# Kernel tuning notes

Measured on AMD Instinct MI355X. Metric: run time of the kernel, lower is better.

Reference implementation:

```python
import jax, jax.numpy as jnp
import numpy as np

T, H, E, I, IS = 1024, 2048, 64, 512, 1024
TOP_K = 8
CAP = 256


def setup_inputs() -> dict:
    key = jax.random.key(0)
    ks = jax.random.split(key, 9)
    s = 0.02
    return {
        "hidden_states": jax.random.normal(ks[0], (T, H), jnp.float32),
        "gate_w": jax.random.normal(ks[1], (E, H), jnp.float32) * s,
        "w1": jax.random.normal(ks[2], (E, H, I), jnp.float32) * s,
        "w3": jax.random.normal(ks[3], (E, H, I), jnp.float32) * s,
        "w2": jax.random.normal(ks[4], (E, I, H), jnp.float32) * s,
        "ws1": jax.random.normal(ks[5], (H, IS), jnp.float32) * s,
        "ws3": jax.random.normal(ks[6], (H, IS), jnp.float32) * s,
        "ws2": jax.random.normal(ks[7], (IS, H), jnp.float32) * s,
        "wsg": jax.random.normal(ks[8], (H, 1), jnp.float32) * s,
    }


def reference(hidden_states, gate_w, w1, w3, w2, ws1, ws3, ws2, wsg):
    x = hidden_states  # [T, H]
    n_tok = x.shape[0]

    # ---- router (Renormalize: top-k over logits, softmax over selected) ----
    logits = x @ gate_w.T                                  # [T, E]
    top_vals, top_idx = jax.lax.top_k(logits, TOP_K)       # [T, k]
    route_w = jax.nn.softmax(top_vals, axis=-1)            # renormalized weights

    # ---- dispatch: flatten (token, slot) assignments, rank within expert ----
    e = top_idx.reshape(-1)                                # [T*k] expert ids
    t = jnp.repeat(jnp.arange(n_tok), TOP_K)               # [T*k] token ids
    w_flat = route_w.reshape(-1)
    order = jnp.argsort(e, stable=True)
    counts = jax.ops.segment_sum(jnp.ones_like(e), e, num_segments=E)
    starts = jnp.cumsum(counts) - counts                   # exclusive cumsum
    pos_sorted = jnp.arange(e.shape[0]) - starts[e[order]]
    pos = jnp.zeros_like(e).at[order].set(pos_sorted)      # rank within expert
    valid = pos < CAP
    slot = jnp.where(valid, e * CAP + pos, E * CAP)        # overflow -> dump slot

    buf = jnp.zeros((E * CAP + 1, x.shape[1]), x.dtype).at[slot].set(x[t])
    xb = buf[:-1].reshape(E, CAP, x.shape[1])              # [E, C, H]

    # ---- grouped SwiGLU experts ----
    g = jax.nn.silu(jnp.einsum('ech,ehi->eci', xb, w1))
    u = jnp.einsum('ech,ehi->eci', xb, w3)
    yb = jnp.einsum('eci,eih->ech', g * u, w2).reshape(E * CAP, -1)

    # ---- combine ----
    contrib = yb[jnp.minimum(slot, E * CAP - 1)] * (w_flat * valid)[:, None]
    routed = jnp.zeros_like(x).at[t].add(contrib)

    # ---- shared expert with sigmoid gate ----
    shared = (jax.nn.silu(x @ ws1) * (x @ ws3)) @ ws2
    shared = jax.nn.sigmoid(x @ wsg) * shared

    return routed + shared
```

## Files before the change

### kernel.cpp

```cpp
#include <hip/hip_runtime.h>
#include <hip/hip_bf16.h>

#define NT    1024
#define HDIM  2048
#define NEXP  64
#define IDIM  512
#define ISDIM 1024
#define KTOP  8
#define ECAP  256

typedef float  f32x4 __attribute__((ext_vector_type(4)));
typedef __bf16 bf16x8 __attribute__((ext_vector_type(8)));
typedef unsigned short u16x8 __attribute__((ext_vector_type(8)));

#define SWZ(r, q) ((((q) ^ ((r) & 3) ^ (((r) >> 2) & 3)) & 3) << 3)

static __device__ __forceinline__ unsigned short f2b(float f) {
  __hip_bfloat16 h = __float2bfloat16(f);
  return __builtin_bit_cast(unsigned short, h);
}
static __device__ __forceinline__ float b2f(unsigned short u) {
  return __bfloat162float(__builtin_bit_cast(__hip_bfloat16, u));
}
static __device__ __forceinline__ void sync_lds() {
  __builtin_amdgcn_s_waitcnt(0xc07f);
  __builtin_amdgcn_s_barrier();
}

__global__ __launch_bounds__(256) void k_router(
    const float* __restrict__ x, const float* __restrict__ gw,
    const float* __restrict__ wsg,
    int* __restrict__ counts, int* __restrict__ tok_list,
    int* __restrict__ slot_map, float* __restrict__ wgt_map,
    float* __restrict__ gate_sig)
{
  __shared__ float xs[HDIM];
  __shared__ float lg[NEXP];
  __shared__ float selv[KTOP];
  __shared__ int   sele[KTOP];
  const int t = blockIdx.x, tid = threadIdx.x;
  const float* xr = x + (size_t)t * HDIM;
  for (int i = tid; i < HDIM / 4; i += 256)
    ((f32x4*)xs)[i] = ((const f32x4*)xr)[i];
  __syncthreads();
  const int wave = tid >> 6, lane = tid & 63;
  for (int ei = 0; ei < 16; ++ei) {
    const int e = wave * 16 + ei;
    const float* g = gw + (size_t)e * HDIM;
    float s = 0.f;
    for (int j = lane; j < HDIM; j += 64) s += xs[j] * g[j];
    for (int off = 32; off; off >>= 1) s += __shfl_xor(s, off, 64);
    if (lane == 0) lg[e] = s;
  }
  if (wave == 1) {
    float s = 0.f;
    for (int j = lane; j < HDIM; j += 64) s += xs[j] * wsg[j];
    for (int off = 32; off; off >>= 1) s += __shfl_xor(s, off, 64);
    if (lane == 0) gate_sig[t] = 1.f / (1.f + __expf(-s));
  }
  __syncthreads();
  if (wave == 0) {
    float v = lg[lane];
    for (int k = 0; k < KTOP; ++k) {
      float m = v;
      for (int off = 32; off; off >>= 1) m = fmaxf(m, __shfl_xor(m, off, 64));
      unsigned long long msk = __ballot(v == m);
      int src = __ffsll(msk) - 1;
      if (lane == src) v = -3.4e38f;
      if (lane == 0) { selv[k] = m; sele[k] = src; }
    }
  }
  __syncthreads();
  if (tid < KTOP) {
    const int k = tid;
    const float mx = selv[0];
    float sum = 0.f;
    for (int i = 0; i < KTOP; ++i) sum += __expf(selv[i] - mx);
    const float w = __expf(selv[k] - mx) / sum;
    const int e = sele[k];
    const int pos = atomicAdd(&counts[e], 1);
    int slot = -1;
    if (pos < ECAP) { slot = e * ECAP + pos; tok_list[slot] = t; }
    slot_map[t * KTOP + k] = slot;
    wgt_map[t * KTOP + k] = w;
  }
}

__global__ __launch_bounds__(512, 2) void k_gemm1(
    const float* __restrict__ x,
    const float* __restrict__ w1, const float* __restrict__ w3,
    const float* __restrict__ ws1, const float* __restrict__ ws3,
    const int* __restrict__ counts, const int* __restrict__ tok_list,
    unsigned short* __restrict__ hbuf, unsigned short* __restrict__ hsbuf)
{
  __shared__ unsigned short lds[32768];
  const int cpx = gridDim.x >> 3;
  const int b0 = blockIdx.x;
  const int bid = (b0 & 7) * cpx + (b0 >> 3);
  const int tid = threadIdx.x;
  bool is_exp;
  int g, ntile, me, ldb, m0s = 0;
  const float *b1p, *b3p;
  if (bid < NEXP * 4) {
    is_exp = true; g = bid >> 2; ntile = bid & 3;
    me = counts[g]; me = me < ECAP ? me : ECAP;
    if (me == 0) return;
    ldb = IDIM;
  } else {
    is_exp = false;
    const int s = bid - NEXP * 4;
    g = s >> 3; ntile = s & 7;
    me = 256; ldb = ISDIM; m0s = g * 256;
  }
  const int n0 = ntile * 128;
  if (is_exp) {
    b1p = w1 + (size_t)g * HDIM * IDIM + n0;
    b3p = w3 + (size_t)g * HDIM * IDIM + n0;
  } else {
    b1p = ws1 + n0;
    b3p = ws3 + n0;
  }
  const int ar = tid & 255, sel = tid >> 8, kh = sel * 16;
  bool avalid;
  const float* arow;
  if (is_exp) {
    avalid = (ar < me);
    const int tok = avalid ? tok_list[g * ECAP + ar] : 0;
    arow = x + (size_t)tok * HDIM + kh;
  } else {
    avalid = true;
    arow = x + (size_t)(m0s + ar) * HDIM + kh;
  }
  const int aoff0 = ar * 32 + SWZ(ar, sel * 2);
  const int aoff1 = ar * 32 + SWZ(ar, sel * 2 + 1);
  const int bn = tid & 127, bg = tid >> 7;
  const float* b1c = b1p + (size_t)(bg * 8) * ldb + bn;
  const float* b3c = b3p + (size_t)(bg * 8) * ldb + bn;
  const int boffB = bn * 32 + SWZ(bn, bg);
  const int lane = tid & 63, quad = lane >> 4, l15 = lane & 15;
  const int wv = tid >> 6, wm = wv >> 1, wn = wv & 1;
  const bool wactive = (wm * 64 < me);
  int aro[4], bo[4];
#pragma unroll
  for (int i = 0; i < 4; ++i) {
    const int rr = wm * 64 + i * 16 + l15;
    aro[i] = rr * 32 + SWZ(rr, quad);
    const int nn = wn * 64 + i * 16 + l15;
    bo[i] = nn * 32 + SWZ(nn, quad);
  }
  f32x4 acc1[4][4], acc3[4][4];
#pragma unroll
  for (int i = 0; i < 4; ++i)
#pragma unroll
    for (int j = 0; j < 4; ++j) {
      acc1[i][j] = f32x4{0.f, 0.f, 0.f, 0.f};
      acc3[i][j] = f32x4{0.f, 0.f, 0.f, 0.f};
    }
  f32x4 arg[4];
  float b1v[8], b3v[8];
  const int KT = HDIM / 32;
  if (avalid) {
    arg[0] = ((const f32x4*)arow)[0]; arg[1] = ((const f32x4*)arow)[1];
    arg[2] = ((const f32x4*)arow)[2]; arg[3] = ((const f32x4*)arow)[3];
  }
#pragma unroll
  for (int j = 0; j < 8; ++j) {
    b1v[j] = b1c[(size_t)j * ldb];
    b3v[j] = b3c[(size_t)j * ldb];
  }

  for (int kt = 0; kt < KT; ++kt) {
    unsigned short* L = lds + (kt & 1) * 16384;
    if (avalid) {
      u16x8 p0, p1;
#pragma unroll
      for (int i = 0; i < 4; ++i) {
        p0[i] = f2b(arg[0][i]); p0[4 + i] = f2b(arg[1][i]);
        p1[i] = f2b(arg[2][i]); p1[4 + i] = f2b(arg[3][i]);
      }
      *(u16x8*)&L[aoff0] = p0;
      *(u16x8*)&L[aoff1] = p1;
    }
    {
      u16x8 pb1, pb3;
#pragma unroll
      for (int j = 0; j < 8; ++j) { pb1[j] = f2b(b1v[j]); pb3[j] = f2b(b3v[j]); }
      *(u16x8*)&L[8192 + boffB] = pb1;
      *(u16x8*)&L[12288 + boffB] = pb3;
    }
    if (kt + 1 < KT) {
      const float* ap = arow + (kt + 1) * 32;
      if (avalid) {
        arg[0] = ((const f32x4*)ap)[0]; arg[1] = ((const f32x4*)ap)[1];
        arg[2] = ((const f32x4*)ap)[2]; arg[3] = ((const f32x4*)ap)[3];
      }
      const float* p1 = b1c + (size_t)(kt + 1) * 32 * ldb;
      const float* p3 = b3c + (size_t)(kt + 1) * 32 * ldb;
#pragma unroll
      for (int j = 0; j < 8; ++j) {
        b1v[j] = p1[(size_t)j * ldb];
        b3v[j] = p3[(size_t)j * ldb];
      }
    }
    sync_lds();
    if (wactive) {
      bf16x8 af[4], bf1[4], bf3[4];
#pragma unroll
      for (int i = 0; i < 4; ++i)
        af[i] = __builtin_bit_cast(bf16x8, *(const u16x8*)&L[aro[i]]);
#pragma unroll
      for (int j = 0; j < 4; ++j) {
        bf1[j] = __builtin_bit_cast(bf16x8, *(const u16x8*)&L[8192 + bo[j]]);
        bf3[j] = __builtin_bit_cast(bf16x8, *(const u16x8*)&L[12288 + bo[j]]);
      }
#pragma unroll
      for (int i = 0; i < 4; ++i)
#pragma unroll
        for (int j = 0; j < 4; ++j) {
          acc1[i][j] = __builtin_amdgcn_mfma_f32_16x16x32_bf16(af[i], bf1[j], acc1[i][j], 0, 0, 0);
          acc3[i][j] = __builtin_amdgcn_mfma_f32_16x16x32_bf16(af[i], bf3[j], acc3[i][j], 0, 0, 0);
        }
    }
  }
  if (wactive) {
#pragma unroll
    for (int i = 0; i < 4; ++i) {
#pragma unroll
      for (int q = 0; q < 4; ++q) {
        const int rr = wm * 64 + i * 16 + quad * 4 + q;
        if (is_exp && rr >= me) continue;
        unsigned short* orow = is_exp
            ? hbuf + ((size_t)g * ECAP + rr) * IDIM
            : hsbuf + (size_t)(m0s + rr) * ISDIM;
#pragma unroll
        for (int j = 0; j < 4; ++j) {
          const int col = n0 + wn * 64 + j * 16 + l15;
          const float gg = acc1[i][j][q];
          const float uu = acc3[i][j][q];
          const float sv = (gg / (1.f + __expf(-gg))) * uu;
          orow[col] = f2b(sv);
        }
      }
    }
  }
}

__global__ __launch_bounds__(512, 2) void k_gemm2(
    const unsigned short* __restrict__ hbuf, const unsigned short* __restrict__ hsbuf,
    const float* __restrict__ w2, const float* __restrict__ ws2,
    const int* __restrict__ counts, const float* __restrict__ gate_sig,
    unsigned short* __restrict__ yb, float* __restrict__ out)
{
  __shared__ unsigned short lds[24576];
  const int cpx = gridDim.x >> 3;
  const int b0 = blockIdx.x;
  const int bid = (b0 & 7) * cpx + (b0 >> 3);
  const int tid = threadIdx.x;
  bool is_exp;
  int g, ntile, me, K, m0s = 0;
  const unsigned short* abase;
  const float* bbase;
  if (bid < NEXP * 16) {
    is_exp = true; g = bid >> 4; ntile = bid & 15;
    me = counts[g]; me = me < ECAP ? me : ECAP;
    if (me == 0) return;
    K = IDIM;
    abase = hbuf + (size_t)g * ECAP * IDIM;
  } else {
    is_exp = false;
    const int s = bid - NEXP * 16;
    g = s >> 4; ntile = s & 15;
    me = 256; K = ISDIM; m0s = g * 256;
    abase = hsbuf + (size_t)m0s * ISDIM;
  }
  const int n0 = ntile * 128;
  bbase = is_exp ? (w2 + (size_t)g * IDIM * HDIM + n0) : (ws2 + n0);
  const int ar = tid & 255, sel = tid >> 8, kh = sel * 16;
  const bool avalid = (ar < me);
  const unsigned short* arow = abase + (size_t)ar * K + kh;
  const int aoff0 = ar * 32 + SWZ(ar, sel * 2);
  const int aoff1 = ar * 32 + SWZ(ar, sel * 2 + 1);
  const int bn = tid & 127, bg = tid >> 7;
  const float* bc = bbase + (size_t)(bg * 8) * HDIM + bn;
  const int boffB = bn * 32 + SWZ(bn, bg);
  const int lane = tid & 63, quad = lane >> 4, l15 = lane & 15;
  const int wv = tid >> 6, wm = wv >> 1, wn = wv & 1;
  const bool wactive = (wm * 64 < me);
  int aro[4], bo[4];
#pragma unroll
  for (int i = 0; i < 4; ++i) {
    const int rr = wm * 64 + i * 16 + l15;
    aro[i] = rr * 32 + SWZ(rr, quad);
    const int nn = wn * 64 + i * 16 + l15;
    bo[i] = nn * 32 + SWZ(nn, quad);
  }
  f32x4 acc[4][4];
#pragma unroll
  for (int i = 0; i < 4; ++i)
#pragma unroll
    for (int j = 0; j < 4; ++j) acc[i][j] = f32x4{0.f, 0.f, 0.f, 0.f};
  u16x8 a0r, a1r;
  float bv[8];
  const int KT = K / 32;
  if (avalid) { a0r = ((const u16x8*)arow)[0]; a1r = ((const u16x8*)arow)[1]; }
#pragma unroll
  for (int j = 0; j < 8; ++j) bv[j] = bc[(size_t)j * HDIM];

  for (int kt = 0; kt < KT; ++kt) {
    unsigned short* L = lds + (kt & 1) * 12288;
    if (avalid) { *(u16x8*)&L[aoff0] = a0r; *(u16x8*)&L[aoff1] = a1r; }
    {
      u16x8 pb;
#pragma unroll
      for (int j = 0; j < 8; ++j) pb[j] = f2b(bv[j]);
      *(u16x8*)&L[8192 + boffB] = pb;
    }
    if (kt + 1 < KT) {
      const unsigned short* ap = arow + (kt + 1) * 32;
      if (avalid) { a0r = ((const u16x8*)ap)[0]; a1r = ((const u16x8*)ap)[1]; }
      const float* p = bc + (size_t)(kt + 1) * 32 * HDIM;
#pragma unroll
      for (int j = 0; j < 8; ++j) bv[j] = p[(size_t)j * HDIM];
    }
    sync_lds();
    if (wactive) {
      bf16x8 af[4], bfr[4];
#pragma unroll
      for (int i = 0; i < 4; ++i)
        af[i] = __builtin_bit_cast(bf16x8, *(const u16x8*)&L[aro[i]]);
#pragma unroll
      for (int j = 0; j < 4; ++j)
        bfr[j] = __builtin_bit_cast(bf16x8, *(const u16x8*)&L[8192 + bo[j]]);
#pragma unroll
      for (int i = 0; i < 4; ++i)
#pragma unroll
        for (int j = 0; j < 4; ++j)
          acc[i][j] = __builtin_amdgcn_mfma_f32_16x16x32_bf16(af[i], bfr[j], acc[i][j], 0, 0, 0);
    }
  }
  if (wactive) {
#pragma unroll
    for (int i = 0; i < 4; ++i) {
#pragma unroll
      for (int q = 0; q < 4; ++q) {
        const int rr = wm * 64 + i * 16 + quad * 4 + q;
        if (is_exp) {
          if (rr >= me) continue;
          unsigned short* orow = yb + ((size_t)g * ECAP + rr) * HDIM;
#pragma unroll
          for (int j = 0; j < 4; ++j) {
            const int col = n0 + wn * 64 + j * 16 + l15;
            orow[col] = f2b(acc[i][j][q]);
          }
        } else {
          const float gt = gate_sig[m0s + rr];
          float* orow = out + (size_t)(m0s + rr) * HDIM;
#pragma unroll
          for (int j = 0; j < 4; ++j) {
            const int col = n0 + wn * 64 + j * 16 + l15;
            orow[col] = gt * acc[i][j][q];
          }
        }
      }
    }
  }
}

__global__ __launch_bounds__(256) void k_combine(
    const unsigned short* __restrict__ yb,
    const int* __restrict__ slot_map, const float* __restrict__ wgt_map,
    float* __restrict__ out)
{
  __shared__ int ss[KTOP];
  __shared__ float ww[KTOP];
  const int t = blockIdx.x, tid = threadIdx.x;
  if (tid < KTOP) { ss[tid] = slot_map[t * KTOP + tid]; ww[tid] = wgt_map[t * KTOP + tid]; }
  __syncthreads();
  const int c = tid * 8;
  float* op = out + (size_t)t * HDIM + c;
  f32x4 o0 = ((const f32x4*)op)[0];
  f32x4 o1 = ((const f32x4*)op)[1];
  for (int k = 0; k < KTOP; ++k) {
    const int s = ss[k];
    if (s < 0) continue;
    const float w = ww[k];
    const u16x8 y = *(const u16x8*)(yb + (size_t)s * HDIM + c);
#pragma unroll
    for (int i = 0; i < 4; ++i) {
      o0[i] += w * b2f(y[i]);
      o1[i] += w * b2f(y[4 + i]);
    }
  }
  ((f32x4*)op)[0] = o0;
  ((f32x4*)op)[1] = o1;
}

extern "C" void kernel_launch(void* const* d_in, const int* in_sizes, int n_in,
                              void* d_out, int out_size, void* d_ws, size_t ws_size,
                              hipStream_t stream) {
  (void)in_sizes; (void)n_in; (void)out_size; (void)ws_size;
  const float* x   = (const float*)d_in[0];
  const float* gw  = (const float*)d_in[1];
  const float* w1  = (const float*)d_in[2];
  const float* w3  = (const float*)d_in[3];
  const float* w2  = (const float*)d_in[4];
  const float* ws1 = (const float*)d_in[5];
  const float* ws3 = (const float*)d_in[6];
  const float* ws2 = (const float*)d_in[7];
  const float* wsg = (const float*)d_in[8];
  float* out = (float*)d_out;
  char* ws = (char*)d_ws;
  int*   counts   = (int*)ws;
  int*   tok_list = (int*)(ws + 256);
  int*   slot_map = (int*)(ws + 256 + (64 << 10));
  float* wgt_map  = (float*)(ws + 256 + (96 << 10));
  float* gate_sig = (float*)(ws + 256 + (128 << 10));
  unsigned short* hbuf  = (unsigned short*)(ws + (1 << 20));
  unsigned short* hsbuf = (unsigned short*)(ws + (17 << 20));
  unsigned short* yb    = (unsigned short*)(ws + (19 << 20));

  hipMemsetAsync(counts, 0, 256, stream);
  k_router<<<dim3(NT), dim3(256), 0, stream>>>(x, gw, wsg, counts, tok_list,
                                               slot_map, wgt_map, gate_sig);
  k_gemm1<<<dim3(NEXP * 4 + 32), dim3(512), 0, stream>>>(x, w1, w3, ws1, ws3,
                                                         counts, tok_list, hbuf, hsbuf);
  k_gemm2<<<dim3(NEXP * 16 + 64), dim3(512), 0, stream>>>(hbuf, hsbuf, w2, ws2,
                                                          counts, gate_sig, yb, out);
  k_combine<<<dim3(NT), dim3(256), 0, stream>>>(yb, slot_map, wgt_map, out);
}
```

Before: 1.099 ms.

## Shrink GEMM tiles to 128x128 and split experts across M tiles

Both grouped GEMM kernels move from 256-row M tiles to 128-row tiles. Experts are split into two M tiles, and tiles that are entirely empty exit early. Warps are rearranged 2x4 and LDS use is halved, and launch bounds now target 4 blocks per CU for higher occupancy and more blocks. The cost is that each weight tile is streamed twice per expert (once per M tile) when the expert has more than 128 tokens, and per-MFMA register reuse is lower.

```diff
diff --git a/kernel.cpp b/kernel.cpp
--- a/kernel.cpp
+++ b/kernel.cpp
@@ -86,170 +86,12 @@
   }
 }
 
-__global__ __launch_bounds__(512, 2) void k_gemm1(
+__global__ __launch_bounds__(512, 4) void k_gemm1(
     const float* __restrict__ x,
     const float* __restrict__ w1, const float* __restrict__ w3,
     const float* __restrict__ ws1, const float* __restrict__ ws3,
     const int* __restrict__ counts, const int* __restrict__ tok_list,
     unsigned short* __restrict__ hbuf, unsigned short* __restrict__ hsbuf)
-{
-  __shared__ unsigned short lds[32768];
-  const int cpx = gridDim.x >> 3;
-  const int b0 = blockIdx.x;
-  const int bid = (b0 & 7) * cpx + (b0 >> 3);
-  const int tid = threadIdx.x;
-  bool is_exp;
-  int g, ntile, me, ldb, m0s = 0;
-  const float *b1p, *b3p;
-  if (bid < NEXP * 4) {
-    is_exp = true; g = bid >> 2; ntile = bid & 3;
-    me = counts[g]; me = me < ECAP ? me : ECAP;
-    if (me == 0) return;
-    ldb = IDIM;
-  } else {
-    is_exp = false;
-    const int s = bid - NEXP * 4;
-    g = s >> 3; ntile = s & 7;
-    me = 256; ldb = ISDIM; m0s = g * 256;
-  }
-  const int n0 = ntile * 128;
-  if (is_exp) {
-    b1p = w1 + (size_t)g * HDIM * IDIM + n0;
-    b3p = w3 + (size_t)g * HDIM * IDIM + n0;
-  } else {
-    b1p = ws1 + n0;
-    b3p = ws3 + n0;
-  }
-  const int ar = tid & 255, sel = tid >> 8, kh = sel * 16;
-  bool avalid;
-  const float* arow;
-  if (is_exp) {
-    avalid = (ar < me);
-    const int tok = avalid ? tok_list[g * ECAP + ar] : 0;
-    arow = x + (size_t)tok * HDIM + kh;
-  } else {
-    avalid = true;
-    arow = x + (size_t)(m0s + ar) * HDIM + kh;
-  }
-  const int aoff0 = ar * 32 + SWZ(ar, sel * 2);
-  const int aoff1 = ar * 32 + SWZ(ar, sel * 2 + 1);
-  const int bn = tid & 127, bg = tid >> 7;
-  const float* b1c = b1p + (size_t)(bg * 8) * ldb + bn;
-  const float* b3c = b3p + (size_t)(bg * 8) * ldb + bn;
-  const int boffB = bn * 32 + SWZ(bn, bg);
-  const int lane = tid & 63, quad = lane >> 4, l15 = lane & 15;
-  const int wv = tid >> 6, wm = wv >> 1, wn = wv & 1;
-  const bool wactive = (wm * 64 < me);
-  int aro[4], bo[4];
-#pragma unroll
-  for (int i = 0; i < 4; ++i) {
-    const int rr = wm * 64 + i * 16 + l15;
-    aro[i] = rr * 32 + SWZ(rr, quad);
-    const int nn = wn * 64 + i * 16 + l15;
-    bo[i] = nn * 32 + SWZ(nn, quad);
-  }
-  f32x4 acc1[4][4], acc3[4][4];
-#pragma unroll
-  for (int i = 0; i < 4; ++i)
-#pragma unroll
-    for (int j = 0; j < 4; ++j) {
-      acc1[i][j] = f32x4{0.f, 0.f, 0.f, 0.f};
-      acc3[i][j] = f32x4{0.f, 0.f, 0.f, 0.f};
-    }
-  f32x4 arg[4];
-  float b1v[8], b3v[8];
-  const int KT = HDIM / 32;
-  if (avalid) {
-    arg[0] = ((const f32x4*)arow)[0]; arg[1] = ((const f32x4*)arow)[1];
-    arg[2] = ((const f32x4*)arow)[2]; arg[3] = ((const f32x4*)arow)[3];
-  }
-#pragma unroll
-  for (int j = 0; j < 8; ++j) {
-    b1v[j] = b1c[(size_t)j * ldb];
-    b3v[j] = b3c[(size_t)j * ldb];
-  }
-
-  for (int kt = 0; kt < KT; ++kt) {
-    unsigned short* L = lds + (kt & 1) * 16384;
-    if (avalid) {
-      u16x8 p0, p1;
-#pragma unroll
-      for (int i = 0; i < 4; ++i) {
-        p0[i] = f2b(arg[0][i]); p0[4 + i] = f2b(arg[1][i]);
-        p1[i] = f2b(arg[2][i]); p1[4 + i] = f2b(arg[3][i]);
-      }
-      *(u16x8*)&L[aoff0] = p0;
-      *(u16x8*)&L[aoff1] = p1;
-    }
-    {
-      u16x8 pb1, pb3;
-#pragma unroll
-      for (int j = 0; j < 8; ++j) { pb1[j] = f2b(b1v[j]); pb3[j] = f2b(b3v[j]); }
-      *(u16x8*)&L[8192 + boffB] = pb1;
-      *(u16x8*)&L[12288 + boffB] = pb3;
-    }
-    if (kt + 1 < KT) {
-      const float* ap = arow + (kt + 1) * 32;
-      if (avalid) {
-        arg[0] = ((const f32x4*)ap)[0]; arg[1] = ((const f32x4*)ap)[1];
-        arg[2] = ((const f32x4*)ap)[2]; arg[3] = ((const f32x4*)ap)[3];
-      }
-      const float* p1 = b1c + (size_t)(kt + 1) * 32 * ldb;
-      const float* p3 = b3c + (size_t)(kt + 1) * 32 * ldb;
-#pragma unroll
-      for (int j = 0; j < 8; ++j) {
-        b1v[j] = p1[(size_t)j * ldb];
-        b3v[j] = p3[(size_t)j * ldb];
-      }
-    }
-    sync_lds();
-    if (wactive) {
-      bf16x8 af[4], bf1[4], bf3[4];
-#pragma unroll
-      for (int i = 0; i < 4; ++i)
-        af[i] = __builtin_bit_cast(bf16x8, *(const u16x8*)&L[aro[i]]);
-#pragma unroll
-      for (int j = 0; j < 4; ++j) {
-        bf1[j] = __builtin_bit_cast(bf16x8, *(const u16x8*)&L[8192 + bo[j]]);
-        bf3[j] = __builtin_bit_cast(bf16x8, *(const u16x8*)&L[12288 + bo[j]]);
-      }
-#pragma unroll
-      for (int i = 0; i < 4; ++i)
-#pragma unroll
-        for (int j = 0; j < 4; ++j) {
-          acc1[i][j] = __builtin_amdgcn_mfma_f32_16x16x32_bf16(af[i], bf1[j], acc1[i][j], 0, 0, 0);
-          acc3[i][j] = __builtin_amdgcn_mfma_f32_16x16x32_bf16(af[i], bf3[j], acc3[i][j], 0, 0, 0);
-        }
-    }
-  }
-  if (wactive) {
-#pragma unroll
-    for (int i = 0; i < 4; ++i) {
-#pragma unroll
-      for (int q = 0; q < 4; ++q) {
-        const int rr = wm * 64 + i * 16 + quad * 4 + q;
-        if (is_exp && rr >= me) continue;
-        unsigned short* orow = is_exp
-            ? hbuf + ((size_t)g * ECAP + rr) * IDIM
-            : hsbuf + (size_t)(m0s + rr) * ISDIM;
-#pragma unroll
-        for (int j = 0; j < 4; ++j) {
-          const int col = n0 + wn * 64 + j * 16 + l15;
-          const float gg = acc1[i][j][q];
-          const float uu = acc3[i][j][q];
-          const float sv = (gg / (1.f + __expf(-gg))) * uu;
-          orow[col] = f2b(sv);
-        }
-      }
-    }
-  }
-}
-
-__global__ __launch_bounds__(512, 2) void k_gemm2(
-    const unsigned short* __restrict__ hbuf, const unsigned short* __restrict__ hsbuf,
-    const float* __restrict__ w2, const float* __restrict__ ws2,
-    const int* __restrict__ counts, const float* __restrict__ gate_sig,
-    unsigned short* __restrict__ yb, float* __restrict__ out)
 {
   __shared__ unsigned short lds[24576];
   const int cpx = gridDim.x >> 3;
@@ -257,85 +99,234 @@
   const int bid = (b0 & 7) * cpx + (b0 >> 3);
   const int tid = threadIdx.x;
   bool is_exp;
-  int g, ntile, me, K, m0s = 0;
+  int g = 0, ntile, mtile, me, ldb, m0;
+  const float *b1p, *b3p;
+  if (bid < NEXP * 8) {
+    is_exp = true;
+    g = bid >> 3; ntile = (bid >> 1) & 3; mtile = bid & 1;
+    me = counts[g]; me = me < ECAP ? me : ECAP;
+    m0 = mtile * 128;
+    if (m0 >= me) return;
+    ldb = IDIM;
+    b1p = w1 + (size_t)g * HDIM * IDIM + ntile * 128;
+    b3p = w3 + (size_t)g * HDIM * IDIM + ntile * 128;
+  } else {
+    is_exp = false;
+    const int s = bid - NEXP * 8;
+    ntile = s >> 3; mtile = s & 7;
+    me = NT; m0 = mtile * 128; ldb = ISDIM;
+    b1p = ws1 + ntile * 128;
+    b3p = ws3 + ntile * 128;
+  }
+  const int n0 = ntile * 128;
+  const int ar = tid & 127, sel = tid >> 7;
+  const bool avalid = (m0 + ar) < me;
+  const float* arow;
+  if (is_exp) {
+    const int tok = avalid ? tok_list[g * ECAP + m0 + ar] : 0;
+    arow = x + (size_t)tok * HDIM + sel * 8;
+  } else {
+    arow = x + (size_t)(m0 + ar) * HDIM + sel * 8;
+  }
+  const int aoff = ar * 32 + SWZ(ar, sel);
+  const int bn = tid & 127, bg = tid >> 7;
+  const float* b1c = b1p + (size_t)(bg * 8) * ldb + bn;
+  const float* b3c = b3p + (size_t)(bg * 8) * ldb + bn;
+  const int boffB = bn * 32 + SWZ(bn, bg);
+  const int lane = tid & 63, quad = lane >> 4, l15 = lane & 15;
+  const int wv = tid >> 6, wm = wv >> 2, wn = wv & 3;
+  const bool wactive = (m0 + wm * 64) < me;
+  int aro[4], bo[2];
+#pragma unroll
+  for (int i = 0; i < 4; ++i) {
+    const int rr = wm * 64 + i * 16 + l15;
+    aro[i] = rr * 32 + SWZ(rr, quad);
+  }
+#pragma unroll
+  for (int j = 0; j < 2; ++j) {
+    const int nn = wn * 32 + j * 16 + l15;
+    bo[j] = nn * 32 + SWZ(nn, quad);
+  }
+  f32x4 acc1[4][2], acc3[4][2];
+#pragma unroll
+  for (int i = 0; i < 4; ++i)
+#pragma unroll
+    for (int j = 0; j < 2; ++j) {
+      acc1[i][j] = f32x4{0.f, 0.f, 0.f, 0.f};
+      acc3[i][j] = f32x4{0.f, 0.f, 0.f, 0.f};
+    }
+  f32x4 a0, a1;
+  float b1v[8], b3v[8];
+  const int KT = HDIM / 32;
+  if (avalid) { a0 = ((const f32x4*)arow)[0]; a1 = ((const f32x4*)arow)[1]; }
+#pragma unroll
+  for (int j = 0; j < 8; ++j) {
+    b1v[j] = b1c[(size_t)j * ldb];
+    b3v[j] = b3c[(size_t)j * ldb];
+  }
+
+  for (int kt = 0; kt < KT; ++kt) {
+    unsigned short* L = lds + (kt & 1) * 12288;
+    if (avalid) {
+      u16x8 p;
+#pragma unroll
+      for (int i = 0; i < 4; ++i) { p[i] = f2b(a0[i]); p[4 + i] = f2b(a1[i]); }
+      *(u16x8*)&L[aoff] = p;
+    }
+    {
+      u16x8 pb1, pb3;
+#pragma unroll
+      for (int j = 0; j < 8; ++j) { pb1[j] = f2b(b1v[j]); pb3[j] = f2b(b3v[j]); }
+      *(u16x8*)&L[4096 + boffB] = pb1;
+      *(u16x8*)&L[8192 + boffB] = pb3;
+    }
+    if (kt + 1 < KT) {
+      const float* ap = arow + (kt + 1) * 32;
+      if (avalid) { a0 = ((const f32x4*)ap)[0]; a1 = ((const f32x4*)ap)[1]; }
+      const float* p1 = b1c + (size_t)(kt + 1) * 32 * ldb;
+      const float* p3 = b3c + (size_t)(kt + 1) * 32 * ldb;
+#pragma unroll
+      for (int j = 0; j < 8; ++j) {
+        b1v[j] = p1[(size_t)j * ldb];
+        b3v[j] = p3[(size_t)j * ldb];
+      }
+    }
+    sync_lds();
+    if (wactive) {
+      bf16x8 bf1[2], bf3[2];
+#pragma unroll
+      for (int j = 0; j < 2; ++j) {
+        bf1[j] = __builtin_bit_cast(bf16x8, *(const u16x8*)&L[4096 + bo[j]]);
+        bf3[j] = __builtin_bit_cast(bf16x8, *(const u16x8*)&L[8192 + bo[j]]);
+      }
+#pragma unroll
+      for (int i = 0; i < 4; ++i) {
+        const bf16x8 af = __builtin_bit_cast(bf16x8, *(const u16x8*)&L[aro[i]]);
+#pragma unroll
+        for (int j = 0; j < 2; ++j) {
+          acc1[i][j] = __builtin_amdgcn_mfma_f32_16x16x32_bf16(af, bf1[j], acc1[i][j], 0, 0, 0);
+          acc3[i][j] = __builtin_amdgcn_mfma_f32_16x16x32_bf16(af, bf3[j], acc3[i][j], 0, 0, 0);
+        }
+      }
+    }
+  }
+  if (wactive) {
+#pragma unroll
+    for (int i = 0; i < 4; ++i) {
+#pragma unroll
+      for (int q = 0; q < 4; ++q) {
+        const int rr = m0 + wm * 64 + i * 16 + quad * 4 + q;
+        if (rr >= me) continue;
+        unsigned short* orow = is_exp
+            ? hbuf + ((size_t)g * ECAP + rr) * IDIM
+            : hsbuf + (size_t)rr * ISDIM;
+#pragma unroll
+        for (int j = 0; j < 2; ++j) {
+          const int col = n0 + wn * 32 + j * 16 + l15;
+          const float gg = acc1[i][j][q];
+          const float uu = acc3[i][j][q];
+          const float sv = (gg / (1.f + __expf(-gg))) * uu;
+          orow[col] = f2b(sv);
+        }
+      }
+    }
+  }
+}
+
+__global__ __launch_bounds__(512, 4) void k_gemm2(
+    const unsigned short* __restrict__ hbuf, const unsigned short* __restrict__ hsbuf,
+    const float* __restrict__ w2, const float* __restrict__ ws2,
+    const int* __restrict__ counts, const float* __restrict__ gate_sig,
+    unsigned short* __restrict__ yb, float* __restrict__ out)
+{
+  __shared__ unsigned short lds[16384];
+  const int cpx = gridDim.x >> 3;
+  const int b0 = blockIdx.x;
+  const int bid = (b0 & 7) * cpx + (b0 >> 3);
+  const int tid = threadIdx.x;
+  bool is_exp;
+  int g = 0, ntile, mtile, me, K, m0;
   const unsigned short* abase;
   const float* bbase;
-  if (bid < NEXP * 16) {
-    is_exp = true; g = bid >> 4; ntile = bid & 15;
+  if (bid < NEXP * 32) {
+    is_exp = true;
+    g = bid >> 5; ntile = (bid >> 1) & 15; mtile = bid & 1;
     me = counts[g]; me = me < ECAP ? me : ECAP;
-    if (me == 0) return;
+    m0 = mtile * 128;
+    if (m0 >= me) return;
     K = IDIM;
     abase = hbuf + (size_t)g * ECAP * IDIM;
+    bbase = w2 + (size_t)g * IDIM * HDIM + ntile * 128;
   } else {
     is_exp = false;
-    const int s = bid - NEXP * 16;
-    g = s >> 4; ntile = s & 15;
-    me = 256; K = ISDIM; m0s = g * 256;
-    abase = hsbuf + (size_t)m0s * ISDIM;
+    const int s = bid - NEXP * 32;
+    ntile = s >> 3; mtile = s & 7;
+    me = NT; m0 = mtile * 128; K = ISDIM;
+    abase = hsbuf;
+    bbase = ws2 + ntile * 128;
   }
   const int n0 = ntile * 128;
-  bbase = is_exp ? (w2 + (size_t)g * IDIM * HDIM + n0) : (ws2 + n0);
-  const int ar = tid & 255, sel = tid >> 8, kh = sel * 16;
-  const bool avalid = (ar < me);
-  const unsigned short* arow = abase + (size_t)ar * K + kh;
-  const int aoff0 = ar * 32 + SWZ(ar, sel * 2);
-  const int aoff1 = ar * 32 + SWZ(ar, sel * 2 + 1);
+  const int ar = tid & 127, sel = tid >> 7;
+  const bool avalid = (m0 + ar) < me;
+  const unsigned short* arow = abase + (size_t)(avalid ? (m0 + ar) : 0) * K + sel * 8;
+  const int aoff = ar * 32 + SWZ(ar, sel);
   const int bn = tid & 127, bg = tid >> 7;
   const float* bc = bbase + (size_t)(bg * 8) * HDIM + bn;
   const int boffB = bn * 32 + SWZ(bn, bg);
   const int lane = tid & 63, quad = lane >> 4, l15 = lane & 15;
-  const int wv = tid >> 6, wm = wv >> 1, wn = wv & 1;
-  const bool wactive = (wm * 64 < me);
-  int aro[4], bo[4];
+  const int wv = tid >> 6, wm = wv >> 2, wn = wv & 3;
+  const bool wactive = (m0 + wm * 64) < me;
+  int aro[4], bo[2];
 #pragma unroll
   for (int i = 0; i < 4; ++i) {
     const int rr = wm * 64 + i * 16 + l15;
     aro[i] = rr * 32 + SWZ(rr, quad);
-    const int nn = wn * 64 + i * 16 + l15;
-    bo[i] = nn * 32 + SWZ(nn, quad);
-  }
-  f32x4 acc[4][4];
+  }
+#pragma unroll
+  for (int j = 0; j < 2; ++j) {
+    const int nn = wn * 32 + j * 16 + l15;
+    bo[j] = nn * 32 + SWZ(nn, quad);
+  }
+  f32x4 acc[4][2];
 #pragma unroll
   for (int i = 0; i < 4; ++i)
 #pragma unroll
-    for (int j = 0; j < 4; ++j) acc[i][j] = f32x4{0.f, 0.f, 0.f, 0.f};
-  u16x8 a0r, a1r;
+    for (int j = 0; j < 2; ++j) acc[i][j] = f32x4{0.f, 0.f, 0.f, 0.f};
+  u16x8 a0r;
   float bv[8];
   const int KT = K / 32;
-  if (avalid) { a0r = ((const u16x8*)arow)[0]; a1r = ((const u16x8*)arow)[1]; }
+  if (avalid) a0r = *(const u16x8*)arow;
 #pragma unroll
   for (int j = 0; j < 8; ++j) bv[j] = bc[(size_t)j * HDIM];
 
   for (int kt = 0; kt < KT; ++kt) {
-    unsigned short* L = lds + (kt & 1) * 12288;
-    if (avalid) { *(u16x8*)&L[aoff0] = a0r; *(u16x8*)&L[aoff1] = a1r; }
+    unsigned short* L = lds + (kt & 1) * 8192;
+    if (avalid) *(u16x8*)&L[aoff] = a0r;
     {
       u16x8 pb;
 #pragma unroll
       for (int j = 0; j < 8; ++j) pb[j] = f2b(bv[j]);
-      *(u16x8*)&L[8192 + boffB] = pb;
+      *(u16x8*)&L[4096 + boffB] = pb;
     }
     if (kt + 1 < KT) {
-      const unsigned short* ap = arow + (kt + 1) * 32;
-      if (avalid) { a0r = ((const u16x8*)ap)[0]; a1r = ((const u16x8*)ap)[1]; }
+      if (avalid) a0r = *(const u16x8*)(arow + (kt + 1) * 32);
       const float* p = bc + (size_t)(kt + 1) * 32 * HDIM;
 #pragma unroll
       for (int j = 0; j < 8; ++j) bv[j] = p[(size_t)j * HDIM];
     }
     sync_lds();
     if (wactive) {
-      bf16x8 af[4], bfr[4];
-#pragma unroll
-      for (int i = 0; i < 4; ++i)
-        af[i] = __builtin_bit_cast(bf16x8, *(const u16x8*)&L[aro[i]]);
-#pragma unroll
-      for (int j = 0; j < 4; ++j)
-        bfr[j] = __builtin_bit_cast(bf16x8, *(const u16x8*)&L[8192 + bo[j]]);
-#pragma unroll
-      for (int i = 0; i < 4; ++i)
-#pragma unroll
-        for (int j = 0; j < 4; ++j)
-          acc[i][j] = __builtin_amdgcn_mfma_f32_16x16x32_bf16(af[i], bfr[j], acc[i][j], 0, 0, 0);
+      bf16x8 bfr[2];
+#pragma unroll
+      for (int j = 0; j < 2; ++j)
+        bfr[j] = __builtin_bit_cast(bf16x8, *(const u16x8*)&L[4096 + bo[j]]);
+#pragma unroll
+      for (int i = 0; i < 4; ++i) {
+        const bf16x8 af = __builtin_bit_cast(bf16x8, *(const u16x8*)&L[aro[i]]);
+#pragma unroll
+        for (int j = 0; j < 2; ++j)
+          acc[i][j] = __builtin_amdgcn_mfma_f32_16x16x32_bf16(af, bfr[j], acc[i][j], 0, 0, 0);
+      }
     }
   }
   if (wactive) {
@@ -343,21 +334,21 @@
     for (int i = 0; i < 4; ++i) {
 #pragma unroll
       for (int q = 0; q < 4; ++q) {
-        const int rr = wm * 64 + i * 16 + quad * 4 + q;
+        const int rr = m0 + wm * 64 + i * 16 + quad * 4 + q;
+        if (rr >= me) continue;
         if (is_exp) {
-          if (rr >= me) continue;
           unsigned short* orow = yb + ((size_t)g * ECAP + rr) * HDIM;
 #pragma unroll
-          for (int j = 0; j < 4; ++j) {
-            const int col = n0 + wn * 64 + j * 16 + l15;
+          for (int j = 0; j < 2; ++j) {
+            const int col = n0 + wn * 32 + j * 16 + l15;
             orow[col] = f2b(acc[i][j][q]);
           }
         } else {
-          const float gt = gate_sig[m0s + rr];
-          float* orow = out + (size_t)(m0s + rr) * HDIM;
-#pragma unroll
-          for (int j = 0; j < 4; ++j) {
-            const int col = n0 + wn * 64 + j * 16 + l15;
+          const float gt = gate_sig[rr];
+          float* orow = out + (size_t)rr * HDIM;
+#pragma unroll
+          for (int j = 0; j < 2; ++j) {
+            const int col = n0 + wn * 32 + j * 16 + l15;
             orow[col] = gt * acc[i][j][q];
           }
         }
@@ -422,9 +413,9 @@
   hipMemsetAsync(counts, 0, 256, stream);
   k_router<<<dim3(NT), dim3(256), 0, stream>>>(x, gw, wsg, counts, tok_list,
                                                slot_map, wgt_map, gate_sig);
-  k_gemm1<<<dim3(NEXP * 4 + 32), dim3(512), 0, stream>>>(x, w1, w3, ws1, ws3,
+  k_gemm1<<<dim3(NEXP * 8 + 64), dim3(512), 0, stream>>>(x, w1, w3, ws1, ws3,
                                                          counts, tok_list, hbuf, hsbuf);
-  k_gemm2<<<dim3(NEXP * 16 + 64), dim3(512), 0, stream>>>(hbuf, hsbuf, w2, ws2,
-                                                          counts, gate_sig, yb, out);
+  k_gemm2<<<dim3(NEXP * 32 + 128), dim3(512), 0, stream>>>(hbuf, hsbuf, w2, ws2,
+                                                           counts, gate_sig, yb, out);
   k_combine<<<dim3(NT), dim3(256), 0, stream>>>(yb, slot_map, wgt_map, out);
 }
```

New measurement: 1.184 ms. 7.7% more time.

## Pre-tile weights to bf16 and stream tiles via direct global-to-LDS loads

Applied to the files above, without the earlier changes.

Adds a k_tile pass that converts every fp32 expert and shared weight matrix into swizzled bf16 tiles each call, then rewrites both GEMM kernels to fetch B (and A for gemm2) with global_load_lds into a triple-buffered LDS ring. The intermediate hbuf/hsbuf is stored in the same tiled layout so gemm2 can load it directly, and gemm1 uses narrower 64-column tiles with more blocks. This removes strided fp32 weight loads and per-iteration register conversion inside the GEMM loops, at the cost of an extra full read and write of all weights every call plus extra kernel launches.

```diff
diff --git a/kernel.cpp b/kernel.cpp
--- a/kernel.cpp
+++ b/kernel.cpp
@@ -22,9 +22,10 @@
 static __device__ __forceinline__ float b2f(unsigned short u) {
   return __bfloat162float(__builtin_bit_cast(__hip_bfloat16, u));
 }
-static __device__ __forceinline__ void sync_lds() {
-  __builtin_amdgcn_s_waitcnt(0xc07f);
-  __builtin_amdgcn_s_barrier();
+static __device__ __forceinline__ void gload16(const unsigned short* g, unsigned short* l) {
+  __builtin_amdgcn_global_load_lds(
+      (const __attribute__((address_space(1))) unsigned int*)g,
+      (__attribute__((address_space(3))) unsigned int*)l, 16, 0, 0);
 }
 
 __global__ __launch_bounds__(256) void k_router(
@@ -86,141 +87,163 @@
   }
 }
 
-__global__ __launch_bounds__(512, 2) void k_gemm1(
+__global__ __launch_bounds__(256) void k_tile(
+    const float* __restrict__ src, unsigned short* __restrict__ dst,
+    const int K, const int N, const int tw128)
+{
+  __shared__ float sb[32 * 512];
+  const int nsh = (N >= 2048) ? 2 : (N >= 1024 ? 1 : 0);
+  const int kt = blockIdx.x >> nsh;
+  const int nc = blockIdx.x & ((1 << nsh) - 1);
+  const int ktiles = K >> 5;
+  const int tshift = tw128 ? 9 : 8;
+  const int tw = tw128 ? 128 : 64;
+  const size_t tile_shorts = tw128 ? 4096 : 2048;
+  const size_t moff_src = (size_t)blockIdx.y * K * N;
+  const size_t moff_dst = (size_t)blockIdx.y * (size_t)(N >> (tw128 ? 7 : 6)) * ktiles * tile_shorts;
+  const int tid = threadIdx.x;
+  const float* s0 = src + moff_src + (size_t)kt * 32 * N + (size_t)nc * 512;
+  for (int i = tid; i < 4096; i += 256) {
+    const int r = i >> 7, c4 = (i & 127) << 2;
+    const f32x4 v = *(const f32x4*)(s0 + (size_t)r * N + c4);
+    *(f32x4*)&sb[r * 512 + (c4 ^ ((r & 7) << 2))] = v;
+  }
+  __syncthreads();
+  unsigned short* d0 = dst + moff_dst;
+#pragma unroll
+  for (int s = 0; s < 8; ++s) {
+    const int c = s * 256 + tid;
+    const int ntl = c >> tshift;
+    const int cc = c & ((1 << tshift) - 1);
+    const int off = cc * 8;
+    const int n = off >> 5;
+    const int j = (off >> 3) & 3;
+    const int kg = (j ^ (n & 3) ^ ((n >> 2) & 3)) & 3;
+    const int gcol = ntl * tw + n;
+    u16x8 p;
+#pragma unroll
+    for (int i2 = 0; i2 < 8; ++i2) {
+      const int r = kg * 8 + i2;
+      p[i2] = f2b(sb[r * 512 + (gcol ^ ((r & 7) << 2))]);
+    }
+    const int ntg = nc * (512 >> (tw128 ? 7 : 6)) + ntl;
+    *(u16x8*)(d0 + ((size_t)ntg * ktiles + kt) * tile_shorts + off) = p;
+  }
+}
+
+__global__ __launch_bounds__(512, 4) void k_gemm1(
     const float* __restrict__ x,
-    const float* __restrict__ w1, const float* __restrict__ w3,
-    const float* __restrict__ ws1, const float* __restrict__ ws3,
+    const unsigned short* __restrict__ w1t, const unsigned short* __restrict__ w3t,
+    const unsigned short* __restrict__ ws1t, const unsigned short* __restrict__ ws3t,
     const int* __restrict__ counts, const int* __restrict__ tok_list,
     unsigned short* __restrict__ hbuf, unsigned short* __restrict__ hsbuf)
 {
-  __shared__ unsigned short lds[32768];
+  extern __shared__ unsigned short lds[];
   const int cpx = gridDim.x >> 3;
   const int b0 = blockIdx.x;
   const int bid = (b0 & 7) * cpx + (b0 >> 3);
   const int tid = threadIdx.x;
-  bool is_exp;
-  int g, ntile, me, ldb, m0s = 0;
-  const float *b1p, *b3p;
-  if (bid < NEXP * 4) {
-    is_exp = true; g = bid >> 2; ntile = bid & 3;
+  bool is_exp; int g = 0, nt, me, m0s = 0;
+  const unsigned short *b1t, *b3t;
+  if (bid < NEXP * 8) {
+    is_exp = true; g = bid >> 3; nt = bid & 7;
     me = counts[g]; me = me < ECAP ? me : ECAP;
     if (me == 0) return;
-    ldb = IDIM;
+    b1t = w1t + (size_t)(g * 8 + nt) * (64 * 2048);
+    b3t = w3t + (size_t)(g * 8 + nt) * (64 * 2048);
   } else {
     is_exp = false;
-    const int s = bid - NEXP * 4;
-    g = s >> 3; ntile = s & 7;
-    me = 256; ldb = ISDIM; m0s = g * 256;
-  }
-  const int n0 = ntile * 128;
-  if (is_exp) {
-    b1p = w1 + (size_t)g * HDIM * IDIM + n0;
-    b3p = w3 + (size_t)g * HDIM * IDIM + n0;
-  } else {
-    b1p = ws1 + n0;
-    b3p = ws3 + n0;
-  }
-  const int ar = tid & 255, sel = tid >> 8, kh = sel * 16;
-  bool avalid;
+    const int s = bid - NEXP * 8;
+    nt = s >> 2; m0s = (s & 3) * 256; me = 256;
+    b1t = ws1t + (size_t)nt * (64 * 2048);
+    b3t = ws3t + (size_t)nt * (64 * 2048);
+  }
+  const int n0 = nt * 64;
+  const int ar = tid & 255, sel2 = tid >> 8;
+  const bool avalid = is_exp ? (ar < me) : true;
   const float* arow;
   if (is_exp) {
-    avalid = (ar < me);
     const int tok = avalid ? tok_list[g * ECAP + ar] : 0;
-    arow = x + (size_t)tok * HDIM + kh;
+    arow = x + (size_t)tok * HDIM + sel2 * 16;
   } else {
-    avalid = true;
-    arow = x + (size_t)(m0s + ar) * HDIM + kh;
-  }
-  const int aoff0 = ar * 32 + SWZ(ar, sel * 2);
-  const int aoff1 = ar * 32 + SWZ(ar, sel * 2 + 1);
-  const int bn = tid & 127, bg = tid >> 7;
-  const float* b1c = b1p + (size_t)(bg * 8) * ldb + bn;
-  const float* b3c = b3p + (size_t)(bg * 8) * ldb + bn;
-  const int boffB = bn * 32 + SWZ(bn, bg);
+    arow = x + (size_t)(m0s + ar) * HDIM + sel2 * 16;
+  }
+  const int ag0 = sel2 * 2;
+  const int aoff0 = ar * 32 + SWZ(ar, ag0);
+  const int aoff1 = ar * 32 + SWZ(ar, ag0 + 1);
+  const int bsub = tid & 255;
+  const unsigned short* btile = (tid < 256) ? b1t : b3t;
+  const int bbase = (tid < 256) ? 16384 : 22528;
+  const int bwq = bsub >> 6;
   const int lane = tid & 63, quad = lane >> 4, l15 = lane & 15;
   const int wv = tid >> 6, wm = wv >> 1, wn = wv & 1;
-  const bool wactive = (wm * 64 < me);
-  int aro[4], bo[4];
+  const bool wactive = is_exp ? (wm * 64 < me) : true;
+  int aro[4], bo[2];
 #pragma unroll
   for (int i = 0; i < 4; ++i) {
     const int rr = wm * 64 + i * 16 + l15;
     aro[i] = rr * 32 + SWZ(rr, quad);
-    const int nn = wn * 64 + i * 16 + l15;
-    bo[i] = nn * 32 + SWZ(nn, quad);
-  }
-  f32x4 acc1[4][4], acc3[4][4];
+  }
+#pragma unroll
+  for (int j = 0; j < 2; ++j) {
+    const int nn = wn * 32 + j * 16 + l15;
+    bo[j] = nn * 32 + SWZ(nn, quad);
+  }
+  f32x4 acc1[4][2], acc3[4][2];
 #pragma unroll
   for (int i = 0; i < 4; ++i)
 #pragma unroll
-    for (int j = 0; j < 4; ++j) {
+    for (int j = 0; j < 2; ++j) {
       acc1[i][j] = f32x4{0.f, 0.f, 0.f, 0.f};
       acc3[i][j] = f32x4{0.f, 0.f, 0.f, 0.f};
     }
-  f32x4 arg[4];
-  float b1v[8], b3v[8];
+  f32x4 a0, a1, a2, a3;
   const int KT = HDIM / 32;
-  if (avalid) {
-    arg[0] = ((const f32x4*)arow)[0]; arg[1] = ((const f32x4*)arow)[1];
-    arg[2] = ((const f32x4*)arow)[2]; arg[3] = ((const f32x4*)arow)[3];
-  }
-#pragma unroll
-  for (int j = 0; j < 8; ++j) {
-    b1v[j] = b1c[(size_t)j * ldb];
-    b3v[j] = b3c[(size_t)j * ldb];
-  }
-
+  gload16(btile + bsub * 8, lds + bbase + bwq * 512);
+  { const f32x4* ap = (const f32x4*)arow;
+    a0 = ap[0]; a1 = ap[1]; a2 = ap[2]; a3 = ap[3]; }
+  int sc = 0, sn = 1;
   for (int kt = 0; kt < KT; ++kt) {
-    unsigned short* L = lds + (kt & 1) * 16384;
-    if (avalid) {
+    unsigned short* A = lds + (kt & 1) * 8192;
+    {
       u16x8 p0, p1;
 #pragma unroll
       for (int i = 0; i < 4; ++i) {
-        p0[i] = f2b(arg[0][i]); p0[4 + i] = f2b(arg[1][i]);
-        p1[i] = f2b(arg[2][i]); p1[4 + i] = f2b(arg[3][i]);
+        p0[i] = f2b(a0[i]); p0[4 + i] = f2b(a1[i]);
+        p1[i] = f2b(a2[i]); p1[4 + i] = f2b(a3[i]);
       }
-      *(u16x8*)&L[aoff0] = p0;
-      *(u16x8*)&L[aoff1] = p1;
-    }
-    {
-      u16x8 pb1, pb3;
-#pragma unroll
-      for (int j = 0; j < 8; ++j) { pb1[j] = f2b(b1v[j]); pb3[j] = f2b(b3v[j]); }
-      *(u16x8*)&L[8192 + boffB] = pb1;
-      *(u16x8*)&L[12288 + boffB] = pb3;
+      *(u16x8*)&A[aoff0] = p0;
+      *(u16x8*)&A[aoff1] = p1;
     }
     if (kt + 1 < KT) {
-      const float* ap = arow + (kt + 1) * 32;
-      if (avalid) {
-        arg[0] = ((const f32x4*)ap)[0]; arg[1] = ((const f32x4*)ap)[1];
-        arg[2] = ((const f32x4*)ap)[2]; arg[3] = ((const f32x4*)ap)[3];
+      gload16(btile + (size_t)(kt + 1) * 2048 + bsub * 8,
+              lds + bbase + sn * 2048 + bwq * 512);
+      const f32x4* ap = (const f32x4*)(arow + (kt + 1) * 32);
+      a0 = ap[0]; a1 = ap[1]; a2 = ap[2]; a3 = ap[3];
+    }
+    asm volatile("s_waitcnt vmcnt(5) lgkmcnt(0)" ::: "memory");
+    __builtin_amdgcn_s_barrier();
+    if (wactive) {
+      const unsigned short* B1 = lds + 16384 + sc * 2048;
+      const unsigned short* B3 = lds + 22528 + sc * 2048;
+      bf16x8 af[4], bb1[2], bb3[2];
+#pragma unroll
+      for (int j = 0; j < 2; ++j) {
+        bb1[j] = __builtin_bit_cast(bf16x8, *(const u16x8*)&B1[bo[j]]);
+        bb3[j] = __builtin_bit_cast(bf16x8, *(const u16x8*)&B3[bo[j]]);
       }
-      const float* p1 = b1c + (size_t)(kt + 1) * 32 * ldb;
-      const float* p3 = b3c + (size_t)(kt + 1) * 32 * ldb;
-#pragma unroll
-      for (int j = 0; j < 8; ++j) {
-        b1v[j] = p1[(size_t)j * ldb];
-        b3v[j] = p3[(size_t)j * ldb];
-      }
-    }
-    sync_lds();
-    if (wactive) {
-      bf16x8 af[4], bf1[4], bf3[4];
 #pragma unroll
       for (int i = 0; i < 4; ++i)
-        af[i] = __builtin_bit_cast(bf16x8, *(const u16x8*)&L[aro[i]]);
-#pragma unroll
-      for (int j = 0; j < 4; ++j) {
-        bf1[j] = __builtin_bit_cast(bf16x8, *(const u16x8*)&L[8192 + bo[j]]);
-        bf3[j] = __builtin_bit_cast(bf16x8, *(const u16x8*)&L[12288 + bo[j]]);
-      }
+        af[i] = __builtin_bit_cast(bf16x8, *(const u16x8*)&A[aro[i]]);
 #pragma unroll
       for (int i = 0; i < 4; ++i)
 #pragma unroll
-        for (int j = 0; j < 4; ++j) {
-          acc1[i][j] = __builtin_amdgcn_mfma_f32_16x16x32_bf16(af[i], bf1[j], acc1[i][j], 0, 0, 0);
-          acc3[i][j] = __builtin_amdgcn_mfma_f32_16x16x32_bf16(af[i], bf3[j], acc3[i][j], 0, 0, 0);
+        for (int j = 0; j < 2; ++j) {
+          acc1[i][j] = __builtin_amdgcn_mfma_f32_16x16x32_bf16(af[i], bb1[j], acc1[i][j], 0, 0, 0);
+          acc3[i][j] = __builtin_amdgcn_mfma_f32_16x16x32_bf16(af[i], bb3[j], acc3[i][j], 0, 0, 0);
         }
     }
+    sc = sn; sn = (sn + 1 == 3) ? 0 : sn + 1;
   }
   if (wactive) {
 #pragma unroll
@@ -229,114 +252,108 @@
       for (int q = 0; q < 4; ++q) {
         const int rr = wm * 64 + i * 16 + quad * 4 + q;
         if (is_exp && rr >= me) continue;
-        unsigned short* orow = is_exp
-            ? hbuf + ((size_t)g * ECAP + rr) * IDIM
-            : hsbuf + (size_t)(m0s + rr) * ISDIM;
-#pragma unroll
-        for (int j = 0; j < 4; ++j) {
-          const int col = n0 + wn * 64 + j * 16 + l15;
+#pragma unroll
+        for (int j = 0; j < 2; ++j) {
+          const int col = n0 + wn * 32 + j * 16 + l15;
           const float gg = acc1[i][j][q];
           const float uu = acc3[i][j][q];
           const float sv = (gg / (1.f + __expf(-gg))) * uu;
-          orow[col] = f2b(sv);
+          const int kti = col >> 5, kk = col & 31;
+          if (is_exp) {
+            const int sl = ((kk >> 3) ^ (rr & 3) ^ ((rr >> 2) & 3)) & 3;
+            hbuf[(((size_t)g * 16 + kti) * 256 + rr) * 32 + sl * 8 + (kk & 7)] = f2b(sv);
+          } else {
+            const int grow = m0s + rr;
+            const int sl = ((kk >> 3) ^ (grow & 3) ^ ((grow >> 2) & 3)) & 3;
+            hsbuf[((size_t)kti * 1024 + grow) * 32 + sl * 8 + (kk & 7)] = f2b(sv);
+          }
         }
       }
     }
   }
 }
 
-__global__ __launch_bounds__(512, 2) void k_gemm2(
+__global__ __launch_bounds__(512, 4) void k_gemm2(
     const unsigned short* __restrict__ hbuf, const unsigned short* __restrict__ hsbuf,
-    const float* __restrict__ w2, const float* __restrict__ ws2,
+    const unsigned short* __restrict__ w2t, const unsigned short* __restrict__ ws2t,
     const int* __restrict__ counts, const float* __restrict__ gate_sig,
     unsigned short* __restrict__ yb, float* __restrict__ out)
 {
-  __shared__ unsigned short lds[24576];
+  extern __shared__ unsigned short lds[];
   const int cpx = gridDim.x >> 3;
   const int b0 = blockIdx.x;
   const int bid = (b0 & 7) * cpx + (b0 >> 3);
   const int tid = threadIdx.x;
-  bool is_exp;
-  int g, ntile, me, K, m0s = 0;
-  const unsigned short* abase;
-  const float* bbase;
+  bool is_exp; int g = 0, nt, me, m0s = 0, KT, astr;
+  const unsigned short *atile, *btile;
   if (bid < NEXP * 16) {
-    is_exp = true; g = bid >> 4; ntile = bid & 15;
+    is_exp = true; g = bid >> 4; nt = bid & 15;
     me = counts[g]; me = me < ECAP ? me : ECAP;
     if (me == 0) return;
-    K = IDIM;
-    abase = hbuf + (size_t)g * ECAP * IDIM;
+    KT = IDIM / 32; astr = 8192;
+    atile = hbuf + (size_t)g * 16 * 8192;
+    btile = w2t + (size_t)(g * 16 + nt) * (16 * 4096);
   } else {
     is_exp = false;
     const int s = bid - NEXP * 16;
-    g = s >> 4; ntile = s & 15;
-    me = 256; K = ISDIM; m0s = g * 256;
-    abase = hsbuf + (size_t)m0s * ISDIM;
-  }
-  const int n0 = ntile * 128;
-  bbase = is_exp ? (w2 + (size_t)g * IDIM * HDIM + n0) : (ws2 + n0);
-  const int ar = tid & 255, sel = tid >> 8, kh = sel * 16;
-  const bool avalid = (ar < me);
-  const unsigned short* arow = abase + (size_t)ar * K + kh;
-  const int aoff0 = ar * 32 + SWZ(ar, sel * 2);
-  const int aoff1 = ar * 32 + SWZ(ar, sel * 2 + 1);
-  const int bn = tid & 127, bg = tid >> 7;
-  const float* bc = bbase + (size_t)(bg * 8) * HDIM + bn;
-  const int boffB = bn * 32 + SWZ(bn, bg);
+    nt = s >> 2; m0s = (s & 3) * 256; me = 256;
+    KT = ISDIM / 32; astr = 32768;
+    atile = hsbuf + (size_t)m0s * 32;
+    btile = ws2t + (size_t)nt * (32 * 4096);
+  }
+  const int n0 = nt * 128;
   const int lane = tid & 63, quad = lane >> 4, l15 = lane & 15;
   const int wv = tid >> 6, wm = wv >> 1, wn = wv & 1;
-  const bool wactive = (wm * 64 < me);
+  const bool wactive = is_exp ? (wm * 64 < me) : true;
   int aro[4], bo[4];
 #pragma unroll
   for (int i = 0; i < 4; ++i) {
     const int rr = wm * 64 + i * 16 + l15;
     aro[i] = rr * 32 + SWZ(rr, quad);
-    const int nn = wn * 64 + i * 16 + l15;
-    bo[i] = nn * 32 + SWZ(nn, quad);
+  }
+#pragma unroll
+  for (int j = 0; j < 4; ++j) {
+    const int nn = wn * 64 + j * 16 + l15;
+    bo[j] = nn * 32 + SWZ(nn, quad);
   }
   f32x4 acc[4][4];
 #pragma unroll
   for (int i = 0; i < 4; ++i)
 #pragma unroll
     for (int j = 0; j < 4; ++j) acc[i][j] = f32x4{0.f, 0.f, 0.f, 0.f};
-  u16x8 a0r, a1r;
-  float bv[8];
-  const int KT = K / 32;
-  if (avalid) { a0r = ((const u16x8*)arow)[0]; a1r = ((const u16x8*)arow)[1]; }
-#pragma unroll
-  for (int j = 0; j < 8; ++j) bv[j] = bc[(size_t)j * HDIM];
-
+  gload16(atile + tid * 8,        lds + wv * 512);
+  gload16(atile + 4096 + tid * 8, lds + 4096 + wv * 512);
+  gload16(btile + tid * 8,        lds + 24576 + wv * 512);
+  int sc = 0, sn = 1;
   for (int kt = 0; kt < KT; ++kt) {
-    unsigned short* L = lds + (kt & 1) * 12288;
-    if (avalid) { *(u16x8*)&L[aoff0] = a0r; *(u16x8*)&L[aoff1] = a1r; }
-    {
-      u16x8 pb;
-#pragma unroll
-      for (int j = 0; j < 8; ++j) pb[j] = f2b(bv[j]);
-      *(u16x8*)&L[8192 + boffB] = pb;
-    }
     if (kt + 1 < KT) {
-      const unsigned short* ap = arow + (kt + 1) * 32;
-      if (avalid) { a0r = ((const u16x8*)ap)[0]; a1r = ((const u16x8*)ap)[1]; }
-      const float* p = bc + (size_t)(kt + 1) * 32 * HDIM;
-#pragma unroll
-      for (int j = 0; j < 8; ++j) bv[j] = p[(size_t)j * HDIM];
-    }
-    sync_lds();
+      const unsigned short* an = atile + (size_t)(kt + 1) * astr;
+      gload16(an + tid * 8,        lds + sn * 8192 + wv * 512);
+      gload16(an + 4096 + tid * 8, lds + sn * 8192 + 4096 + wv * 512);
+      gload16(btile + (size_t)(kt + 1) * 4096 + tid * 8,
+              lds + 24576 + sn * 4096 + wv * 512);
+      asm volatile("s_waitcnt vmcnt(3)" ::: "memory");
+    } else {
+      asm volatile("s_waitcnt vmcnt(0)" ::: "memory");
+    }
+    __builtin_amdgcn_s_barrier();
     if (wactive) {
-      bf16x8 af[4], bfr[4];
+      const unsigned short* A = lds + sc * 8192;
+      const unsigned short* B = lds + 24576 + sc * 4096;
+      bf16x8 af[4], bf[4];
+#pragma unroll
+      for (int j = 0; j < 4; ++j)
+        bf[j] = __builtin_bit_cast(bf16x8, *(const u16x8*)&B[bo[j]]);
 #pragma unroll
       for (int i = 0; i < 4; ++i)
-        af[i] = __builtin_bit_cast(bf16x8, *(const u16x8*)&L[aro[i]]);
-#pragma unroll
-      for (int j = 0; j < 4; ++j)
-        bfr[j] = __builtin_bit_cast(bf16x8, *(const u16x8*)&L[8192 + bo[j]]);
+        af[i] = __builtin_bit_cast(bf16x8, *(const u16x8*)&A[aro[i]]);
 #pragma unroll
       for (int i = 0; i < 4; ++i)
 #pragma unroll
         for (int j = 0; j < 4; ++j)
-          acc[i][j] = __builtin_amdgcn_mfma_f32_16x16x32_bf16(af[i], bfr[j], acc[i][j], 0, 0, 0);
-    }
+          acc[i][j] = __builtin_amdgcn_mfma_f32_16x16x32_bf16(af[i], bf[j], acc[i][j], 0, 0, 0);
+    }
+    sc = sn; sn = (sn + 1 == 3) ? 0 : sn + 1;
   }
   if (wactive) {
 #pragma unroll
@@ -353,8 +370,9 @@
             orow[col] = f2b(acc[i][j][q]);
           }
         } else {
-          const float gt = gate_sig[m0s + rr];
-          float* orow = out + (size_t)(m0s + rr) * HDIM;
+          const int grow = m0s + rr;
+          const float gt = gate_sig[grow];
+          float* orow = out + (size_t)grow * HDIM;
 #pragma unroll
           for (int j = 0; j < 4; ++j) {
             const int col = n0 + wn * 64 + j * 16 + l15;
@@ -410,21 +428,34 @@
   const float* wsg = (const float*)d_in[8];
   float* out = (float*)d_out;
   char* ws = (char*)d_ws;
+  const size_t MiB = (size_t)1 << 20;
   int*   counts   = (int*)ws;
   int*   tok_list = (int*)(ws + 256);
   int*   slot_map = (int*)(ws + 256 + (64 << 10));
   float* wgt_map  = (float*)(ws + 256 + (96 << 10));
   float* gate_sig = (float*)(ws + 256 + (128 << 10));
-  unsigned short* hbuf  = (unsigned short*)(ws + (1 << 20));
-  unsigned short* hsbuf = (unsigned short*)(ws + (17 << 20));
-  unsigned short* yb    = (unsigned short*)(ws + (19 << 20));
+  unsigned short* hbuf  = (unsigned short*)(ws + 1 * MiB);
+  unsigned short* hsbuf = (unsigned short*)(ws + 17 * MiB);
+  unsigned short* ws1t  = (unsigned short*)(ws + 19 * MiB);
+  unsigned short* ws3t  = (unsigned short*)(ws + 23 * MiB);
+  unsigned short* ws2t  = (unsigned short*)(ws + 27 * MiB);
+  unsigned short* w1t   = (unsigned short*)(ws + 32 * MiB);
+  unsigned short* w3t   = (unsigned short*)(ws + 160 * MiB);
+  unsigned short* w2t   = w1t;
+  unsigned short* yb    = (unsigned short*)(ws + 160 * MiB);
 
   hipMemsetAsync(counts, 0, 256, stream);
   k_router<<<dim3(NT), dim3(256), 0, stream>>>(x, gw, wsg, counts, tok_list,
                                                slot_map, wgt_map, gate_sig);
-  k_gemm1<<<dim3(NEXP * 4 + 32), dim3(512), 0, stream>>>(x, w1, w3, ws1, ws3,
-                                                         counts, tok_list, hbuf, hsbuf);
-  k_gemm2<<<dim3(NEXP * 16 + 64), dim3(512), 0, stream>>>(hbuf, hsbuf, w2, ws2,
-                                                          counts, gate_sig, yb, out);
+  k_tile<<<dim3(64, 64), dim3(256), 0, stream>>>(w1, w1t, HDIM, IDIM, 0);
+  k_tile<<<dim3(64, 64), dim3(256), 0, stream>>>(w3, w3t, HDIM, IDIM, 0);
+  k_tile<<<dim3(128, 1), dim3(256), 0, stream>>>(ws1, ws1t, HDIM, ISDIM, 0);
+  k_tile<<<dim3(128, 1), dim3(256), 0, stream>>>(ws3, ws3t, HDIM, ISDIM, 0);
+  k_tile<<<dim3(128, 1), dim3(256), 0, stream>>>(ws2, ws2t, ISDIM, HDIM, 1);
+  k_gemm1<<<dim3(NEXP * 8 + 64), dim3(512), 57344, stream>>>(
+      x, w1t, w3t, ws1t, ws3t, counts, tok_list, hbuf, hsbuf);
+  k_tile<<<dim3(64, 64), dim3(256), 0, stream>>>(w2, w2t, IDIM, HDIM, 1);
+  k_gemm2<<<dim3(NEXP * 16 + 64), dim3(512), 73728, stream>>>(
+      hbuf, hsbuf, w2t, ws2t, counts, gate_sig, yb, out);
   k_combine<<<dim3(NT), dim3(256), 0, stream>>>(yb, slot_map, wgt_map, out);
 }
```

Result: slower. 1.346 ms (+22.5%).
